# Kernel tuning notes

Hardware: AMD Instinct MI355X
Metric: run time of the kernel (lower is better)

## Reference

```python
import jax, jax.numpy as jnp
import numpy as np

N_NODES = 100000
N_EDGES = 1600000
D = 64


def setup_inputs() -> dict:
    key = jax.random.key(0)
    k0, k1, k2, k3 = jax.random.split(key, 4)
    x = jax.random.normal(k0, (N_NODES, D), dtype=jnp.float32)
    edge_index = jax.random.randint(k1, (2, N_EDGES), 0, N_NODES, dtype=jnp.int64)
    W1 = jax.random.normal(k2, (D, D), dtype=jnp.float32) * 0.1
    b1 = jnp.zeros((D,), dtype=jnp.float32)
    W2 = jax.random.normal(k3, (D, D), dtype=jnp.float32) * 0.1
    b2 = jnp.zeros((D,), dtype=jnp.float32)
    return {"x": x, "edge_index": edge_index, "W1": W1, "b1": b1, "W2": W2, "b2": b2}


def _gcn_layer(x, edge_index, W, b):
    n = x.shape[0]
    h = x @ W  # [N, Dout] -- transform before aggregation (small GEMM)
    loop = jnp.arange(n, dtype=edge_index.dtype)
    src = jnp.concatenate([edge_index[0], loop])
    dst = jnp.concatenate([edge_index[1], loop])
    deg = jax.ops.segment_sum(jnp.ones_like(dst, dtype=h.dtype), dst, num_segments=n)
    dinv = jax.lax.rsqrt(deg)  # deg >= 1 thanks to self loops
    norm = dinv[src] * dinv[dst]  # [E+N]
    msg = h[src] * norm[:, None]  # gather: [E+N, Dout]
    agg = jax.ops.segment_sum(msg, dst, num_segments=n)  # scatter-add
    return agg + b


def reference(x, edge_index, W1, b1, W2, b2):
    # dropout p = 0.0 -> identity
    h = jax.nn.relu(_gcn_layer(x, edge_index, W1, b1))
    h = jax.nn.relu(_gcn_layer(h, edge_index, W2, b2))
    return h
```

## Files before the change

### kernel.cpp

```cpp
#include <hip/hip_runtime.h>
#include <hip/hip_bf16.h>

#define D 64
#define NB_HIST 256
#define MAXBK 512

typedef float vfloat4 __attribute__((ext_vector_type(4)));
typedef short short8 __attribute__((ext_vector_type(8)));
typedef float f32x4 __attribute__((ext_vector_type(4)));

__device__ __forceinline__ unsigned short f2bf(float f) {
    union { float f; unsigned u; } v; v.f = f;
    unsigned r = (v.u + 0x7FFF + ((v.u >> 16) & 1)) >> 16;
    return (unsigned short)r;
}
__device__ __forceinline__ unsigned short bftrunc(float f) {
    union { float f; unsigned u; } v; v.f = f;
    return (unsigned short)(v.u >> 16);
}
__device__ __forceinline__ float bffrom(unsigned short h) {
    union { unsigned u; float f; } v; v.u = ((unsigned)h) << 16; return v.f;
}
__device__ __forceinline__ float bflo(unsigned u) {
    union { unsigned u; float f; } v; v.u = u << 16; return v.f;
}
__device__ __forceinline__ float bfhi(unsigned u) {
    union { unsigned u; float f; } v; v.u = u & 0xFFFF0000u; return v.f;
}

__global__ __launch_bounds__(256) void passA_hist_wfrag(
    const int* __restrict__ dst, int* __restrict__ blockCounts, int E, int per, int NBK,
    const float* __restrict__ W1, const float* __restrict__ W2,
    unsigned short* __restrict__ WfH1, unsigned short* __restrict__ WfL1,
    unsigned short* __restrict__ WfH2, unsigned short* __restrict__ WfL2)
{
    int tid = threadIdx.x;

    if ((int)blockIdx.x < NB_HIST) {
        __shared__ int hist[MAXBK];
        for (int i = tid; i < NBK; i += 256) hist[i] = 0;
        __syncthreads();
        int lo = blockIdx.x * per, hi = min(E, lo + per);
        for (int i = lo + tid * 4; i < hi; i += 1024) {
            if (i + 3 < hi) {
                int4 d4 = *(const int4*)(dst + i);
                atomicAdd(&hist[d4.x >> 8], 1);
                atomicAdd(&hist[d4.y >> 8], 1);
                atomicAdd(&hist[d4.z >> 8], 1);
                atomicAdd(&hist[d4.w >> 8], 1);
            } else {
                for (int k = i; k < hi; ++k) atomicAdd(&hist[dst[k] >> 8], 1);
            }
        }
        __syncthreads();
        for (int i = tid; i < NBK; i += 256)
            blockCounts[(size_t)blockIdx.x * NBK + i] = hist[i];
        return;
    }

    int b = (int)blockIdx.x - NB_HIST;
    const float* Wsrc = (b >> 1) ? W2 : W1;
    unsigned short* fh = (b >> 1) ? WfH2 : WfH1;
    unsigned short* fl = (b >> 1) ? WfL2 : WfL1;
    int combo = (b & 1) * 4 + (tid >> 6);
    int lane = tid & 63;
    int s = combo >> 2, c = combo & 3, g = lane >> 4, rl = lane & 15;
#pragma unroll
    for (int j = 0; j < 8; ++j) {
        float v = Wsrc[(32 * s + 8 * g + j) * D + 16 * c + rl];
        unsigned short h = bftrunc(v);
        fh[combo * 512 + lane * 8 + j] = h;
        fl[combo * 512 + lane * 8 + j] = f2bf(v - bffrom(h));
    }
}

__global__ __launch_bounds__(256) void gemm1_mfma(
    const float* __restrict__ X,
    const unsigned short* __restrict__ WfH, const unsigned short* __restrict__ WfL,
    unsigned short* __restrict__ hn, int N)
{
    int t = threadIdx.x, wave = t >> 6, lane = t & 63;
    int rowBase = (int)blockIdx.x * 64 + wave * 16;
    if (rowBase >= N) return;
    int g = lane >> 4, rl = lane & 15;

    short8 BH[2][4], BL[2][4];
#pragma unroll
    for (int s = 0; s < 2; ++s)
#pragma unroll
        for (int c = 0; c < 4; ++c) {
            BH[s][c] = *(const short8*)(WfH + ((s * 4 + c) * 64 + lane) * 8);
            BL[s][c] = *(const short8*)(WfL + ((s * 4 + c) * 64 + lane) * 8);
        }

    int arow = rowBase + rl; if (arow >= N) arow = N - 1;
    const float* xr = X + (size_t)arow * D;

    f32x4 acc[4];
#pragma unroll
    for (int c = 0; c < 4; ++c) acc[c] = (f32x4){0.f, 0.f, 0.f, 0.f};

#pragma unroll
    for (int s = 0; s < 2; ++s) {
        vfloat4 x0 = *(const vfloat4*)(xr + 32 * s + 8 * g);
        vfloat4 x1 = *(const vfloat4*)(xr + 32 * s + 8 * g + 4);
        short8 ah, al;
#pragma unroll
        for (int j = 0; j < 4; ++j) {
            unsigned short h0 = bftrunc(x0[j]);
            ah[j] = (short)h0; al[j] = (short)f2bf(x0[j] - bffrom(h0));
            unsigned short h1 = bftrunc(x1[j]);
            ah[j + 4] = (short)h1; al[j + 4] = (short)f2bf(x1[j] - bffrom(h1));
        }
#pragma unroll
        for (int c = 0; c < 4; ++c)
            acc[c] = __builtin_amdgcn_mfma_f32_16x16x32_bf16(ah, BH[s][c], acc[c], 0, 0, 0);
#pragma unroll
        for (int c = 0; c < 4; ++c)
            acc[c] = __builtin_amdgcn_mfma_f32_16x16x32_bf16(ah, BL[s][c], acc[c], 0, 0, 0);
#pragma unroll
        for (int c = 0; c < 4; ++c)
            acc[c] = __builtin_amdgcn_mfma_f32_16x16x32_bf16(al, BH[s][c], acc[c], 0, 0, 0);
    }

#pragma unroll
    for (int r = 0; r < 4; ++r) {
        int row = rowBase + g * 4 + r;
        if (row < N) {
            unsigned short* hr = hn + (size_t)row * D + rl;
#pragma unroll
            for (int c = 0; c < 4; ++c) hr[c * 16] = f2bf(acc[c][r]);
        }
    }
}

__global__ __launch_bounds__(256) void scan_cols(
    const int* __restrict__ blockCounts, int* __restrict__ partial,
    int* __restrict__ totals, int NBK)
{
    int wave = threadIdx.x >> 6, lane = threadIdx.x & 63;
    int k = blockIdx.x * 4 + wave;
    if (k >= NBK) return;
    int carry = 0;
    for (int base = 0; base < NB_HIST; base += 64) {
        int b = base + lane;
        int v = blockCounts[(size_t)b * NBK + k];
        int inc = v;
        for (int d = 1; d < 64; d <<= 1) {
            int t = __shfl_up(inc, d, 64);
            if (lane >= d) inc += t;
        }
        partial[(size_t)k * NB_HIST + b] = inc - v + carry;
        carry += __shfl(inc, 63, 64);
    }
    if (lane == 0) totals[k] = carry;
}

__global__ void scan_buckets(const int* __restrict__ totals, int* __restrict__ bofs, int NBK) {
    int lane = threadIdx.x;
    int carry = 0;
    for (int base = 0; base < NBK; base += 64) {
        int i = base + lane;
        int v = (i < NBK) ? totals[i] : 0;
        int inc = v;
        for (int d = 1; d < 64; d <<= 1) {
            int t = __shfl_up(inc, d, 64);
            if (lane >= d) inc += t;
        }
        if (i < NBK) bofs[i] = inc - v + carry;
        carry += __shfl(inc, 63, 64);
    }
}

__global__ __launch_bounds__(256) void passB(
    const int* __restrict__ src, const int* __restrict__ dst,
    const int* __restrict__ bofs, const int* __restrict__ partial,
    int* __restrict__ bucketed, int E, int per, int NBK)
{
    __shared__ int cur[MAXBK];
    int tid = threadIdx.x, b = blockIdx.x;
    for (int i = tid; i < NBK; i += 256)
        cur[i] = bofs[i] + partial[(size_t)i * NB_HIST + b];
    __syncthreads();
    int lo = b * per, hi = min(E, lo + per);
    for (int i = lo + tid * 4; i < hi; i += 1024) {
        if (i + 3 < hi) {
            int4 d4 = *(const int4*)(dst + i);
            int4 s4 = *(const int4*)(src + i);
            int p0 = atomicAdd(&cur[d4.x >> 8], 1);
            int p1 = atomicAdd(&cur[d4.y >> 8], 1);
            int p2 = atomicAdd(&cur[d4.z >> 8], 1);
            int p3 = atomicAdd(&cur[d4.w >> 8], 1);
            bucketed[p0] = (s4.x << 8) | (d4.x & 255);
            bucketed[p1] = (s4.y << 8) | (d4.y & 255);
            bucketed[p2] = (s4.z << 8) | (d4.z & 255);
            bucketed[p3] = (s4.w << 8) | (d4.w & 255);
        } else {
            for (int k = i; k < hi; ++k) {
                int d = dst[k], s = src[k];
                int pos = atomicAdd(&cur[d >> 8], 1);
                bucketed[pos] = (s << 8) | (d & 255);
            }
        }
    }
}

__global__ __launch_bounds__(256) void build_csr_scale(
    const int* __restrict__ bucketed, const int* __restrict__ bofs,
    const int* __restrict__ totals, int* __restrict__ deg, float* __restrict__ dinv,
    int* __restrict__ ofs, int* __restrict__ csr,
    unsigned short* __restrict__ hn, int N)
{
    __shared__ int h[256];
    __shared__ int scn[256];
    __shared__ float sdv[256];
    int tid = threadIdx.x, k = blockIdx.x;
    int e0 = bofs[k], e1 = e0 + totals[k];
    int node = k * 256 + tid;

    h[tid] = 0;
    __syncthreads();
    for (int i = e0 + tid; i < e1; i += 256)
        atomicAdd(&h[bucketed[i] & 255], 1);
    __syncthreads();

    int mydeg = h[tid];
    scn[tid] = mydeg;
    __syncthreads();
    for (int d2 = 1; d2 < 256; d2 <<= 1) {
        int t = (tid >= d2) ? scn[tid - d2] : 0;
        __syncthreads();
        scn[tid] += t;
        __syncthreads();
    }
    int myofs = scn[tid] - mydeg;

    float dv = rsqrtf((float)(mydeg + 1));
    sdv[tid] = dv;
    if (node < N) {
        deg[node]  = mydeg;
        dinv[node] = dv;
        ofs[node]  = e0 + myofs;
    }

    h[tid] = myofs;
    __syncthreads();
    for (int i = e0 + tid; i < e1; i += 256) {
        int v = bucketed[i];
        int pos = atomicAdd(&h[v & 255], 1);
        csr[e0 + pos] = v >> 8;
    }

    __syncthreads();
    int4* hp = (int4*)hn;
    for (int c = tid; c < 2048; c += 256) {
        int r = c >> 3;
        int n2 = k * 256 + r;
        if (n2 < N) {
            float f = sdv[r];
            size_t idx = (size_t)n2 * 8 + (c & 7);
            int4 hv = hp[idx];
            unsigned r0 = (unsigned)f2bf(bflo(hv.x) * f) | ((unsigned)f2bf(bfhi(hv.x) * f) << 16);
            unsigned r1 = (unsigned)f2bf(bflo(hv.y) * f) | ((unsigned)f2bf(bfhi(hv.y) * f) << 16);
            unsigned r2 = (unsigned)f2bf(bflo(hv.z) * f) | ((unsigned)f2bf(bfhi(hv.z) * f) << 16);
            unsigned r3 = (unsigned)f2bf(bflo(hv.w) * f) | ((unsigned)f2bf(bfhi(hv.w) * f) << 16);
            hp[idx] = make_int4((int)r0, (int)r1, (int)r2, (int)r3);
        }
    }
}

__global__ __launch_bounds__(256) void gemm2_mfma(
    const unsigned short* __restrict__ h1b,
    const unsigned short* __restrict__ WfH, const unsigned short* __restrict__ WfL,
    const float* __restrict__ dinv, unsigned short* __restrict__ hn, int N)
{
    int t = threadIdx.x, wave = t >> 6, lane = t & 63;
    int rowBase = (int)blockIdx.x * 64 + wave * 16;
    if (rowBase >= N) return;
    int g = lane >> 4, rl = lane & 15;

    short8 BH[2][4], BL[2][4];
#pragma unroll
    for (int s = 0; s < 2; ++s)
#pragma unroll
        for (int c = 0; c < 4; ++c) {
            BH[s][c] = *(const short8*)(WfH + ((s * 4 + c) * 64 + lane) * 8);
            BL[s][c] = *(const short8*)(WfL + ((s * 4 + c) * 64 + lane) * 8);
        }

    int arow = rowBase + rl; if (arow >= N) arow = N - 1;
    const unsigned short* hr0 = h1b + (size_t)arow * D;

    f32x4 acc[4];
#pragma unroll
    for (int c = 0; c < 4; ++c) acc[c] = (f32x4){0.f, 0.f, 0.f, 0.f};

#pragma unroll
    for (int s = 0; s < 2; ++s) {
        short8 a = *(const short8*)(hr0 + 32 * s + 8 * g);
#pragma unroll
        for (int c = 0; c < 4; ++c)
            acc[c] = __builtin_amdgcn_mfma_f32_16x16x32_bf16(a, BH[s][c], acc[c], 0, 0, 0);
#pragma unroll
        for (int c = 0; c < 4; ++c)
            acc[c] = __builtin_amdgcn_mfma_f32_16x16x32_bf16(a, BL[s][c], acc[c], 0, 0, 0);
    }

#pragma unroll
    for (int r = 0; r < 4; ++r) {
        int row = rowBase + g * 4 + r;
        if (row < N) {
            float dv = dinv[row];
            unsigned short* hw = hn + (size_t)row * D + rl;
#pragma unroll
            for (int c = 0; c < 4; ++c) hw[c * 16] = f2bf(acc[c][r] * dv);
        }
    }
}

template <bool BF16OUT>
__global__ __launch_bounds__(256) void aggregate_relu(
    const int* __restrict__ ofs, const int* __restrict__ deg,
    const int* __restrict__ csr, const unsigned short* __restrict__ hn,
    const float* __restrict__ dinv, const float* __restrict__ bias,
    void* __restrict__ outv, int N)
{
    int t    = blockIdx.x * 256 + threadIdx.x;
    int lane = threadIdx.x & 63;
    int grp  = lane >> 3, sub = lane & 7;
    int node = (t >> 6) * 8 + grp;
    bool live = (node < N);

    const int4* hrow = (const int4*)hn;
    float2 a0 = {0.f, 0.f}, a1 = {0.f, 0.f}, a2 = {0.f, 0.f}, a3 = {0.f, 0.f};

    int s0 = 0, cnt = 0;
    if (live) {
        s0  = ofs[node];
        cnt = deg[node];
        int4 h = hrow[(size_t)node * 8 + sub];
        a0.x += bflo(h.x); a0.y += bfhi(h.x);
        a1.x += bflo(h.y); a1.y += bfhi(h.y);
        a2.x += bflo(h.z); a2.y += bfhi(h.z);
        a3.x += bflo(h.w); a3.y += bfhi(h.w);
    }

    const int* cp = csr + s0;
    int j = 0;
    for (; j + 3 < cnt; j += 4) {
        int sA = cp[j], sB = cp[j + 1], sC = cp[j + 2], sD = cp[j + 3];
        int4 hA = hrow[(size_t)sA * 8 + sub];
        int4 hB = hrow[(size_t)sB * 8 + sub];
        int4 hC = hrow[(size_t)sC * 8 + sub];
        int4 hD = hrow[(size_t)sD * 8 + sub];
        a0.x += bflo(hA.x); a0.y += bfhi(hA.x);
        a1.x += bflo(hA.y); a1.y += bfhi(hA.y);
        a2.x += bflo(hA.z); a2.y += bfhi(hA.z);
        a3.x += bflo(hA.w); a3.y += bfhi(hA.w);
        a0.x += bflo(hB.x); a0.y += bfhi(hB.x);
        a1.x += bflo(hB.y); a1.y += bfhi(hB.y);
        a2.x += bflo(hB.z); a2.y += bfhi(hB.z);
        a3.x += bflo(hB.w); a3.y += bfhi(hB.w);
        a0.x += bflo(hC.x); a0.y += bfhi(hC.x);
        a1.x += bflo(hC.y); a1.y += bfhi(hC.y);
        a2.x += bflo(hC.z); a2.y += bfhi(hC.z);
        a3.x += bflo(hC.w); a3.y += bfhi(hC.w);
        a0.x += bflo(hD.x); a0.y += bfhi(hD.x);
        a1.x += bflo(hD.y); a1.y += bfhi(hD.y);
        a2.x += bflo(hD.z); a2.y += bfhi(hD.z);
        a3.x += bflo(hD.w); a3.y += bfhi(hD.w);
    }
    for (; j < cnt; ++j) {
        int sA = cp[j];
        int4 hA = hrow[(size_t)sA * 8 + sub];
        a0.x += bflo(hA.x); a0.y += bfhi(hA.x);
        a1.x += bflo(hA.y); a1.y += bfhi(hA.y);
        a2.x += bflo(hA.z); a2.y += bfhi(hA.z);
        a3.x += bflo(hA.w); a3.y += bfhi(hA.w);
    }

    if (live) {
        float dw = dinv[node];
        float4 b0 = ((const float4*)bias)[sub * 2];
        float4 b1 = ((const float4*)bias)[sub * 2 + 1];
        float o0 = fmaxf(a0.x * dw + b0.x, 0.f);
        float o1 = fmaxf(a0.y * dw + b0.y, 0.f);
        float o2 = fmaxf(a1.x * dw + b0.z, 0.f);
        float o3 = fmaxf(a1.y * dw + b0.w, 0.f);
        float o4 = fmaxf(a2.x * dw + b1.x, 0.f);
        float o5 = fmaxf(a2.y * dw + b1.y, 0.f);
        float o6 = fmaxf(a3.x * dw + b1.z, 0.f);
        float o7 = fmaxf(a3.y * dw + b1.w, 0.f);
        if (BF16OUT) {
            unsigned r0 = (unsigned)f2bf(o0) | ((unsigned)f2bf(o1) << 16);
            unsigned r1 = (unsigned)f2bf(o2) | ((unsigned)f2bf(o3) << 16);
            unsigned r2 = (unsigned)f2bf(o4) | ((unsigned)f2bf(o5) << 16);
            unsigned r3 = (unsigned)f2bf(o6) | ((unsigned)f2bf(o7) << 16);
            ((int4*)outv)[(size_t)node * 8 + sub] =
                make_int4((int)r0, (int)r1, (int)r2, (int)r3);
        } else {
            float4 v0 = make_float4(o0, o1, o2, o3);
            float4 v1 = make_float4(o4, o5, o6, o7);
            ((float4*)outv)[(size_t)node * 16 + sub * 2]     = v0;
            ((float4*)outv)[(size_t)node * 16 + sub * 2 + 1] = v1;
        }
    }
}


extern "C" void kernel_launch(void* const* d_in, const int* in_sizes, int n_in,
                              void* d_out, int out_size, void* d_ws, size_t ws_size,
                              hipStream_t stream) {
    const float* x   = (const float*)d_in[0];
    const int*   ei  = (const int*)d_in[1];
    const float* W1  = (const float*)d_in[2];
    const float* b1  = (const float*)d_in[3];
    const float* W2  = (const float*)d_in[4];
    const float* b2  = (const float*)d_in[5];

    int N = in_sizes[0] / D;
    int E = in_sizes[1] / 2;
    const int* src = ei;
    const int* dst = ei + E;
    int NBK = (N + 255) >> 8;
    int per = (((E + NB_HIST - 1) / NB_HIST) + 3) & ~3;

    char* ws = (char*)d_ws;
    int*            blockCounts = (int*)(ws + 0x00000000);
    int*            partial     = (int*)(ws + 0x00080000);
    int*            totals      = (int*)(ws + 0x00100000);
    int*            bofs        = (int*)(ws + 0x00110000);
    int*            deg         = (int*)(ws + 0x00120000);
    float*          dinv        = (float*)(ws + 0x00190000);
    int*            ofs         = (int*)(ws + 0x00200000);
    int*            bucketed    = (int*)(ws + 0x00280000);
    int*            csr         = (int*)(ws + 0x00A00000);
    unsigned short* hn          = (unsigned short*)(ws + 0x01100000);
    unsigned short* h1b         = (unsigned short*)(ws + 0x01D80000);
    unsigned short* WfH1        = (unsigned short*)(ws + 0x02A80000);
    unsigned short* WfL1        = WfH1 + 4096;
    unsigned short* WfH2        = WfL1 + 4096;
    unsigned short* WfL2        = WfH2 + 4096;
    float*          outF        = (float*)d_out;

    int nb_G = (N + 63) / 64;
    int nb_A = (N + 31) / 32;

    passA_hist_wfrag<<<NB_HIST + 4, 256, 0, stream>>>(dst, blockCounts, E, per, NBK,
                                                      W1, W2, WfH1, WfL1, WfH2, WfL2);
    gemm1_mfma<<<nb_G, 256, 0, stream>>>(x, WfH1, WfL1, hn, N);
    scan_cols<<<(NBK + 3) / 4, 256, 0, stream>>>(blockCounts, partial, totals, NBK);
    scan_buckets<<<1, 64, 0, stream>>>(totals, bofs, NBK);
    passB<<<NB_HIST, 256, 0, stream>>>(src, dst, bofs, partial, bucketed, E, per, NBK);
    build_csr_scale<<<NBK, 256, 0, stream>>>(bucketed, bofs, totals, deg, dinv, ofs, csr, hn, N);

    aggregate_relu<true><<<nb_A, 256, 0, stream>>>(ofs, deg, csr, hn, dinv, b1, (void*)h1b, N);
    gemm2_mfma<<<nb_G, 256, 0, stream>>>(h1b, WfH2, WfL2, dinv, hn, N);
    aggregate_relu<false><<<nb_A, 256, 0, stream>>>(ofs, deg, csr, hn, dinv, b2, (void*)outF, N);
}
```

Baseline: 221.8 us.

## Fuse layer-1 aggregation with layer-2 GEMM and fold dinv scaling into GEMM1

```diff
diff --git a/kernel.cpp b/kernel.cpp
--- a/kernel.cpp
+++ b/kernel.cpp
@@ -71,66 +71,6 @@
         unsigned short h = bftrunc(v);
         fh[combo * 512 + lane * 8 + j] = h;
         fl[combo * 512 + lane * 8 + j] = f2bf(v - bffrom(h));
-    }
-}
-
-__global__ __launch_bounds__(256) void gemm1_mfma(
-    const float* __restrict__ X,
-    const unsigned short* __restrict__ WfH, const unsigned short* __restrict__ WfL,
-    unsigned short* __restrict__ hn, int N)
-{
-    int t = threadIdx.x, wave = t >> 6, lane = t & 63;
-    int rowBase = (int)blockIdx.x * 64 + wave * 16;
-    if (rowBase >= N) return;
-    int g = lane >> 4, rl = lane & 15;
-
-    short8 BH[2][4], BL[2][4];
-#pragma unroll
-    for (int s = 0; s < 2; ++s)
-#pragma unroll
-        for (int c = 0; c < 4; ++c) {
-            BH[s][c] = *(const short8*)(WfH + ((s * 4 + c) * 64 + lane) * 8);
-            BL[s][c] = *(const short8*)(WfL + ((s * 4 + c) * 64 + lane) * 8);
-        }
-
-    int arow = rowBase + rl; if (arow >= N) arow = N - 1;
-    const float* xr = X + (size_t)arow * D;
-
-    f32x4 acc[4];
-#pragma unroll
-    for (int c = 0; c < 4; ++c) acc[c] = (f32x4){0.f, 0.f, 0.f, 0.f};
-
-#pragma unroll
-    for (int s = 0; s < 2; ++s) {
-        vfloat4 x0 = *(const vfloat4*)(xr + 32 * s + 8 * g);
-        vfloat4 x1 = *(const vfloat4*)(xr + 32 * s + 8 * g + 4);
-        short8 ah, al;
-#pragma unroll
-        for (int j = 0; j < 4; ++j) {
-            unsigned short h0 = bftrunc(x0[j]);
-            ah[j] = (short)h0; al[j] = (short)f2bf(x0[j] - bffrom(h0));
-            unsigned short h1 = bftrunc(x1[j]);
-            ah[j + 4] = (short)h1; al[j + 4] = (short)f2bf(x1[j] - bffrom(h1));
-        }
-#pragma unroll
-        for (int c = 0; c < 4; ++c)
-            acc[c] = __builtin_amdgcn_mfma_f32_16x16x32_bf16(ah, BH[s][c], acc[c], 0, 0, 0);
-#pragma unroll
-        for (int c = 0; c < 4; ++c)
-            acc[c] = __builtin_amdgcn_mfma_f32_16x16x32_bf16(ah, BL[s][c], acc[c], 0, 0, 0);
-#pragma unroll
-        for (int c = 0; c < 4; ++c)
-            acc[c] = __builtin_amdgcn_mfma_f32_16x16x32_bf16(al, BH[s][c], acc[c], 0, 0, 0);
-    }
-
-#pragma unroll
-    for (int r = 0; r < 4; ++r) {
-        int row = rowBase + g * 4 + r;
-        if (row < N) {
-            unsigned short* hr = hn + (size_t)row * D + rl;
-#pragma unroll
-            for (int c = 0; c < 4; ++c) hr[c * 16] = f2bf(acc[c][r]);
-        }
     }
 }
 
@@ -205,15 +145,13 @@
     }
 }
 
-__global__ __launch_bounds__(256) void build_csr_scale(
+__global__ __launch_bounds__(256) void build_csr(
     const int* __restrict__ bucketed, const int* __restrict__ bofs,
     const int* __restrict__ totals, int* __restrict__ deg, float* __restrict__ dinv,
-    int* __restrict__ ofs, int* __restrict__ csr,
-    unsigned short* __restrict__ hn, int N)
+    int* __restrict__ ofs, int* __restrict__ csr, int N)
 {
     __shared__ int h[256];
     __shared__ int scn[256];
-    __shared__ float sdv[256];
     int tid = threadIdx.x, k = blockIdx.x;
     int e0 = bofs[k], e1 = e0 + totals[k];
     int node = k * 256 + tid;
@@ -235,11 +173,9 @@
     }
     int myofs = scn[tid] - mydeg;
 
-    float dv = rsqrtf((float)(mydeg + 1));
-    sdv[tid] = dv;
     if (node < N) {
         deg[node]  = mydeg;
-        dinv[node] = dv;
+        dinv[node] = rsqrtf((float)(mydeg + 1));
         ofs[node]  = e0 + myofs;
     }
 
@@ -250,27 +186,10 @@
         int pos = atomicAdd(&h[v & 255], 1);
         csr[e0 + pos] = v >> 8;
     }
-
-    __syncthreads();
-    int4* hp = (int4*)hn;
-    for (int c = tid; c < 2048; c += 256) {
-        int r = c >> 3;
-        int n2 = k * 256 + r;
-        if (n2 < N) {
-            float f = sdv[r];
-            size_t idx = (size_t)n2 * 8 + (c & 7);
-            int4 hv = hp[idx];
-            unsigned r0 = (unsigned)f2bf(bflo(hv.x) * f) | ((unsigned)f2bf(bfhi(hv.x) * f) << 16);
-            unsigned r1 = (unsigned)f2bf(bflo(hv.y) * f) | ((unsigned)f2bf(bfhi(hv.y) * f) << 16);
-            unsigned r2 = (unsigned)f2bf(bflo(hv.z) * f) | ((unsigned)f2bf(bfhi(hv.z) * f) << 16);
-            unsigned r3 = (unsigned)f2bf(bflo(hv.w) * f) | ((unsigned)f2bf(bfhi(hv.w) * f) << 16);
-            hp[idx] = make_int4((int)r0, (int)r1, (int)r2, (int)r3);
-        }
-    }
-}
-
-__global__ __launch_bounds__(256) void gemm2_mfma(
-    const unsigned short* __restrict__ h1b,
+}
+
+__global__ __launch_bounds__(256) void gemm1_mfma(
+    const float* __restrict__ X,
     const unsigned short* __restrict__ WfH, const unsigned short* __restrict__ WfL,
     const float* __restrict__ dinv, unsigned short* __restrict__ hn, int N)
 {
@@ -289,7 +208,7 @@
         }
 
     int arow = rowBase + rl; if (arow >= N) arow = N - 1;
-    const unsigned short* hr0 = h1b + (size_t)arow * D;
+    const float* xr = X + (size_t)arow * D;
 
     f32x4 acc[4];
 #pragma unroll
@@ -297,13 +216,25 @@
 
 #pragma unroll
     for (int s = 0; s < 2; ++s) {
-        short8 a = *(const short8*)(hr0 + 32 * s + 8 * g);
+        vfloat4 x0 = *(const vfloat4*)(xr + 32 * s + 8 * g);
+        vfloat4 x1 = *(const vfloat4*)(xr + 32 * s + 8 * g + 4);
+        short8 ah, al;
+#pragma unroll
+        for (int j = 0; j < 4; ++j) {
+            unsigned short h0 = bftrunc(x0[j]);
+            ah[j] = (short)h0; al[j] = (short)f2bf(x0[j] - bffrom(h0));
+            unsigned short h1 = bftrunc(x1[j]);
+            ah[j + 4] = (short)h1; al[j + 4] = (short)f2bf(x1[j] - bffrom(h1));
+        }
 #pragma unroll
         for (int c = 0; c < 4; ++c)
-            acc[c] = __builtin_amdgcn_mfma_f32_16x16x32_bf16(a, BH[s][c], acc[c], 0, 0, 0);
+            acc[c] = __builtin_amdgcn_mfma_f32_16x16x32_bf16(ah, BH[s][c], acc[c], 0, 0, 0);
 #pragma unroll
         for (int c = 0; c < 4; ++c)
-            acc[c] = __builtin_amdgcn_mfma_f32_16x16x32_bf16(a, BL[s][c], acc[c], 0, 0, 0);
+            acc[c] = __builtin_amdgcn_mfma_f32_16x16x32_bf16(ah, BL[s][c], acc[c], 0, 0, 0);
+#pragma unroll
+        for (int c = 0; c < 4; ++c)
+            acc[c] = __builtin_amdgcn_mfma_f32_16x16x32_bf16(al, BH[s][c], acc[c], 0, 0, 0);
     }
 
 #pragma unroll
@@ -311,27 +242,30 @@
         int row = rowBase + g * 4 + r;
         if (row < N) {
             float dv = dinv[row];
-            unsigned short* hw = hn + (size_t)row * D + rl;
-#pragma unroll
-            for (int c = 0; c < 4; ++c) hw[c * 16] = f2bf(acc[c][r] * dv);
-        }
-    }
-}
-
-template <bool BF16OUT>
-__global__ __launch_bounds__(256) void aggregate_relu(
+            unsigned short* hr = hn + (size_t)row * D + rl;
+#pragma unroll
+            for (int c = 0; c < 4; ++c) hr[c * 16] = f2bf(acc[c][r] * dv);
+        }
+    }
+}
+
+__global__ __launch_bounds__(256) void agg1_gemm2(
     const int* __restrict__ ofs, const int* __restrict__ deg,
-    const int* __restrict__ csr, const unsigned short* __restrict__ hn,
+    const int* __restrict__ csr, const unsigned short* __restrict__ hnA,
     const float* __restrict__ dinv, const float* __restrict__ bias,
-    void* __restrict__ outv, int N)
-{
-    int t    = blockIdx.x * 256 + threadIdx.x;
-    int lane = threadIdx.x & 63;
+    const unsigned short* __restrict__ WfH, const unsigned short* __restrict__ WfL,
+    unsigned short* __restrict__ hnB, int N)
+{
+    __shared__ unsigned short sH[32 * 72];
+    int tid  = threadIdx.x;
+    int lane = tid & 63, wave = tid >> 6;
     int grp  = lane >> 3, sub = lane & 7;
-    int node = (t >> 6) * 8 + grp;
+    int rowInBlk = wave * 8 + grp;
+    int nodeBase = (int)blockIdx.x * 32;
+    int node = nodeBase + rowInBlk;
     bool live = (node < N);
 
-    const int4* hrow = (const int4*)hn;
+    const int4* hrow = (const int4*)hnA;
     float2 a0 = {0.f, 0.f}, a1 = {0.f, 0.f}, a2 = {0.f, 0.f}, a3 = {0.f, 0.f};
 
     int s0 = 0, cnt = 0;
@@ -379,6 +313,123 @@
         a3.x += bflo(hA.w); a3.y += bfhi(hA.w);
     }
 
+    {
+        float dw = live ? dinv[node] : 0.f;
+        float4 b0 = ((const float4*)bias)[sub * 2];
+        float4 b1 = ((const float4*)bias)[sub * 2 + 1];
+        float o0 = fmaxf(a0.x * dw + b0.x, 0.f);
+        float o1 = fmaxf(a0.y * dw + b0.y, 0.f);
+        float o2 = fmaxf(a1.x * dw + b0.z, 0.f);
+        float o3 = fmaxf(a1.y * dw + b0.w, 0.f);
+        float o4 = fmaxf(a2.x * dw + b1.x, 0.f);
+        float o5 = fmaxf(a2.y * dw + b1.y, 0.f);
+        float o6 = fmaxf(a3.x * dw + b1.z, 0.f);
+        float o7 = fmaxf(a3.y * dw + b1.w, 0.f);
+        unsigned r0 = (unsigned)f2bf(o0) | ((unsigned)f2bf(o1) << 16);
+        unsigned r1 = (unsigned)f2bf(o2) | ((unsigned)f2bf(o3) << 16);
+        unsigned r2 = (unsigned)f2bf(o4) | ((unsigned)f2bf(o5) << 16);
+        unsigned r3 = (unsigned)f2bf(o6) | ((unsigned)f2bf(o7) << 16);
+        *(int4*)&sH[rowInBlk * 72 + sub * 8] = make_int4((int)r0, (int)r1, (int)r2, (int)r3);
+    }
+    __syncthreads();
+
+    if (wave < 2) {
+        int g = lane >> 4, rl = lane & 15;
+        f32x4 acc[4];
+#pragma unroll
+        for (int c = 0; c < 4; ++c) acc[c] = (f32x4){0.f, 0.f, 0.f, 0.f};
+
+#pragma unroll
+        for (int s = 0; s < 2; ++s) {
+            short8 a = *(const short8*)&sH[(wave * 16 + rl) * 72 + 32 * s + 8 * g];
+            short8 BH[4], BL[4];
+#pragma unroll
+            for (int c = 0; c < 4; ++c) {
+                BH[c] = *(const short8*)(WfH + ((s * 4 + c) * 64 + lane) * 8);
+                BL[c] = *(const short8*)(WfL + ((s * 4 + c) * 64 + lane) * 8);
+            }
+#pragma unroll
+            for (int c = 0; c < 4; ++c)
+                acc[c] = __builtin_amdgcn_mfma_f32_16x16x32_bf16(a, BH[c], acc[c], 0, 0, 0);
+#pragma unroll
+            for (int c = 0; c < 4; ++c)
+                acc[c] = __builtin_amdgcn_mfma_f32_16x16x32_bf16(a, BL[c], acc[c], 0, 0, 0);
+        }
+
+#pragma unroll
+        for (int r = 0; r < 4; ++r) {
+            int row = nodeBase + wave * 16 + g * 4 + r;
+            if (row < N) {
+                float dv = dinv[row];
+                unsigned short* hw = hnB + (size_t)row * D + rl;
+#pragma unroll
+                for (int c = 0; c < 4; ++c) hw[c * 16] = f2bf(acc[c][r] * dv);
+            }
+        }
+    }
+}
+
+template <bool BF16OUT>
+__global__ __launch_bounds__(256) void aggregate_relu(
+    const int* __restrict__ ofs, const int* __restrict__ deg,
+    const int* __restrict__ csr, const unsigned short* __restrict__ hn,
+    const float* __restrict__ dinv, const float* __restrict__ bias,
+    void* __restrict__ outv, int N)
+{
+    int t    = blockIdx.x * 256 + threadIdx.x;
+    int lane = threadIdx.x & 63;
+    int grp  = lane >> 3, sub = lane & 7;
+    int node = (t >> 6) * 8 + grp;
+    bool live = (node < N);
+
+    const int4* hrow = (const int4*)hn;
+    float2 a0 = {0.f, 0.f}, a1 = {0.f, 0.f}, a2 = {0.f, 0.f}, a3 = {0.f, 0.f};
+
+    int s0 = 0, cnt = 0;
+    if (live) {
+        s0  = ofs[node];
+        cnt = deg[node];
+        int4 h = hrow[(size_t)node * 8 + sub];
+        a0.x += bflo(h.x); a0.y += bfhi(h.x);
+        a1.x += bflo(h.y); a1.y += bfhi(h.y);
+        a2.x += bflo(h.z); a2.y += bfhi(h.z);
+        a3.x += bflo(h.w); a3.y += bfhi(h.w);
+    }
+
+    const int* cp = csr + s0;
+    int j = 0;
+    for (; j + 3 < cnt; j += 4) {
+        int sA = cp[j], sB = cp[j + 1], sC = cp[j + 2], sD = cp[j + 3];
+        int4 hA = hrow[(size_t)sA * 8 + sub];
+        int4 hB = hrow[(size_t)sB * 8 + sub];
+        int4 hC = hrow[(size_t)sC * 8 + sub];
+        int4 hD = hrow[(size_t)sD * 8 + sub];
+        a0.x += bflo(hA.x); a0.y += bfhi(hA.x);
+        a1.x += bflo(hA.y); a1.y += bfhi(hA.y);
+        a2.x += bflo(hA.z); a2.y += bfhi(hA.z);
+        a3.x += bflo(hA.w); a3.y += bfhi(hA.w);
+        a0.x += bflo(hB.x); a0.y += bfhi(hB.x);
+        a1.x += bflo(hB.y); a1.y += bfhi(hB.y);
+        a2.x += bflo(hB.z); a2.y += bfhi(hB.z);
+        a3.x += bflo(hB.w); a3.y += bfhi(hB.w);
+        a0.x += bflo(hC.x); a0.y += bfhi(hC.x);
+        a1.x += bflo(hC.y); a1.y += bfhi(hC.y);
+        a2.x += bflo(hC.z); a2.y += bfhi(hC.z);
+        a3.x += bflo(hC.w); a3.y += bfhi(hC.w);
+        a0.x += bflo(hD.x); a0.y += bfhi(hD.x);
+        a1.x += bflo(hD.y); a1.y += bfhi(hD.y);
+        a2.x += bflo(hD.z); a2.y += bfhi(hD.z);
+        a3.x += bflo(hD.w); a3.y += bfhi(hD.w);
+    }
+    for (; j < cnt; ++j) {
+        int sA = cp[j];
+        int4 hA = hrow[(size_t)sA * 8 + sub];
+        a0.x += bflo(hA.x); a0.y += bfhi(hA.x);
+        a1.x += bflo(hA.y); a1.y += bfhi(hA.y);
+        a2.x += bflo(hA.z); a2.y += bfhi(hA.z);
+        a3.x += bflo(hA.w); a3.y += bfhi(hA.w);
+    }
+
     if (live) {
         float dw = dinv[node];
         float4 b0 = ((const float4*)bias)[sub * 2];
@@ -435,8 +486,8 @@
     int*            ofs         = (int*)(ws + 0x00200000);
     int*            bucketed    = (int*)(ws + 0x00280000);
     int*            csr         = (int*)(ws + 0x00A00000);
-    unsigned short* hn          = (unsigned short*)(ws + 0x01100000);
-    unsigned short* h1b         = (unsigned short*)(ws + 0x01D80000);
+    unsigned short* hnA         = (unsigned short*)(ws + 0x01100000);
+    unsigned short* hnB         = (unsigned short*)(ws + 0x01D80000);
     unsigned short* WfH1        = (unsigned short*)(ws + 0x02A80000);
     unsigned short* WfL1        = WfH1 + 4096;
     unsigned short* WfH2        = WfL1 + 4096;
@@ -448,13 +499,12 @@
 
     passA_hist_wfrag<<<NB_HIST + 4, 256, 0, stream>>>(dst, blockCounts, E, per, NBK,
                                                       W1, W2, WfH1, WfL1, WfH2, WfL2);
-    gemm1_mfma<<<nb_G, 256, 0, stream>>>(x, WfH1, WfL1, hn, N);
     scan_cols<<<(NBK + 3) / 4, 256, 0, stream>>>(blockCounts, partial, totals, NBK);
     scan_buckets<<<1, 64, 0, stream>>>(totals, bofs, NBK);
     passB<<<NB_HIST, 256, 0, stream>>>(src, dst, bofs, partial, bucketed, E, per, NBK);
-    build_csr_scale<<<NBK, 256, 0, stream>>>(bucketed, bofs, totals, deg, dinv, ofs, csr, hn, N);
-
-    aggregate_relu<true><<<nb_A, 256, 0, stream>>>(ofs, deg, csr, hn, dinv, b1, (void*)h1b, N);
-    gemm2_mfma<<<nb_G, 256, 0, stream>>>(h1b, WfH2, WfL2, dinv, hn, N);
-    aggregate_relu<false><<<nb_A, 256, 0, stream>>>(ofs, deg, csr, hn, dinv, b2, (void*)outF, N);
-}
+    build_csr<<<NBK, 256, 0, stream>>>(bucketed, bofs, totals, deg, dinv, ofs, csr, N);
+
+    gemm1_mfma<<<nb_G, 256, 0, stream>>>(x, WfH1, WfL1, dinv, hnA, N);
+    agg1_gemm2<<<nb_A, 256, 0, stream>>>(ofs, deg, csr, hnA, dinv, b1, WfH2, WfL2, hnB, N);
+    aggregate_relu<false><<<nb_A, 256, 0, stream>>>(ofs, deg, csr, hnB, dinv, b2, (void*)outF, N);
+}
```

Result: faster. 204.3 us (-7.9%).
